# Optimization experiments

Hardware: AMD Instinct MI355X
Metric: run time of the kernel (lower is better)

Reference implementation:

```python
import jax, jax.numpy as jnp
import numpy as np

ALPHA = 0.2  # LeakyReLU slope in GAT
OUT_SLOPE = 0.01  # default nn.LeakyyReLU slope for self.out
B, E, IN_DIM, HID, HEADS = 4, 2048, 32, 18, 3
DH = HID // HEADS  # per-head out dim = 6


def _leaky(x, slope):
    return jnp.where(x > 0, x, slope * x)


def _gat_head(x, adj, W, a):
    # x: [B,E,in], W: [in,dh], a: [2*dh,1]
    h = jnp.einsum('bei,id->bed', x, W)                      # [B,E,dh]
    d = h.shape[-1]
    # score[b,i,j] = leakyrelu(a . concat(h_i, h_j)) = leakyrelu(h_i.a1 + h_j.a2)
    e1 = jnp.einsum('bed,d->be', h, a[:d, 0])
    e2 = jnp.einsum('bed,d->be', h, a[d:, 0])
    score = _leaky(e1[:, :, None] + e2[:, None, :], ALPHA)   # [B,E,E]
    scores = jnp.where(adj == 1.0, score, 0.0)
    logits = jnp.where(adj > 0.0, scores, -30.0)
    att = jax.nn.softmax(logits, axis=2)                     # softmax over j
    # h_prime[b,j,d] = sum_i att[b,i,j] * h[b,i,d]  (torch sums over dim=1)
    h_prime = jnp.einsum('bij,bid->bjd', att, h)
    return jax.nn.elu(h_prime)  # concat=True -> elu


def _gat_multihead(x, adj, Ws, As):
    # Ws: [H,in,dh], As: [H,2*dh,1]
    outs = jax.vmap(lambda W, a: _gat_head(x, adj, W, a))(Ws, As)  # [H,B,E,dh]
    H, b, e, d = outs.shape
    return jnp.moveaxis(outs, 0, 2).reshape(b, e, H * d)  # concat heads last-dim


def _gcn(x, adj2d, W, b):
    return adj2d @ (x @ W) + b


def setup_inputs() -> dict:
    key = jax.random.key(0)
    ks = jax.random.split(key, 16)
    node_input = jax.random.normal(ks[0], (B, E, IN_DIM), jnp.float32)
    uv_filed = jax.random.normal(ks[1], (B, E, IN_DIM), jnp.float32)
    adj = jax.random.randint(ks[2], (B, E, E), 0, 2).astype(jnp.float32)
    s = 0.1
    Wt1 = jax.random.normal(ks[3], (HEADS, IN_DIM, DH), jnp.float32) * s
    at1 = jax.random.normal(ks[4], (HEADS, 2 * DH, 1), jnp.float32) * s
    Wt2 = jax.random.normal(ks[5], (HEADS, IN_DIM, DH), jnp.float32) * s
    at2 = jax.random.normal(ks[6], (HEADS, 2 * DH, 1), jnp.float32) * s
    Wg1 = jax.random.normal(ks[7], (HID, 16), jnp.float32) * s
    bg1 = jnp.zeros((16,), jnp.float32)
    Wg2 = jax.random.normal(ks[8], (16, 2), jnp.float32) * s
    bg2 = jnp.zeros((2,), jnp.float32)
    Wo1 = jax.random.normal(ks[9], (HID, 16), jnp.float32) * s
    bo1 = jnp.zeros((16,), jnp.float32)
    Wo2 = jax.random.normal(ks[10], (16, 2), jnp.float32) * s
    bo2 = jnp.zeros((2,), jnp.float32)
    return dict(node_input=node_input, uv_filed=uv_filed, adj=adj,
                Wt1=Wt1, at1=at1, Wt2=Wt2, at2=at2,
                Wg1=Wg1, bg1=bg1, Wg2=Wg2, bg2=bg2,
                Wo1=Wo1, bo1=bo1, Wo2=Wo2, bo2=bo2)


def reference(node_input, uv_filed, adj, Wt1, at1, Wt2, at2,
              Wg1, bg1, Wg2, bg2, Wo1, bo1, Wo2, bo2):
    h = _gat_multihead(node_input, adj, Wt1, at1)  # [B,E,18]
    o = _gat_multihead(uv_filed, adj, Wt2, at2)    # [B,E,18]
    a0 = adj[0]
    Y = jax.nn.relu(_gcn(h[0], a0, Wg1, bg1))
    O = jax.nn.relu(_gcn(o[0], a0, Wo1, bo1))
    Y = _gcn(Y, a0, Wg2, bg2)
    O = _gcn(O, a0, Wo2, bo2)
    return (jax.nn.log_softmax(Y, axis=1), _leaky(O, OUT_SLOPE))
```

## Files before the change

kernel.cpp:

```cpp
#include <hip/hip_runtime.h>
#include <hip/hip_bf16.h>


__global__ __launch_bounds__(256) void k01(
    const float* __restrict__ adj0, unsigned int* __restrict__ bm,
    const float* __restrict__ node, const float* __restrict__ uv,
    const float* __restrict__ Wt1, const float* __restrict__ at1,
    const float* __restrict__ Wt2, const float* __restrict__ at2,
    float* __restrict__ hcol, float* __restrict__ pack1, float* __restrict__ pack2) {
  int b = blockIdx.x;
  if (b < 512) {
    int lane = threadIdx.x & 63, w = threadIdx.x >> 6;
    int row = b * 4 + w;
    const float* arow = adj0 + (size_t)row * 2048;
#pragma unroll 4
    for (int it = 0; it < 32; ++it) {
      float v = arow[it * 64 + lane];
      unsigned long long mask = __ballot(v == 1.0f);
      if (lane == 0) bm[row * 64 + it * 2] = (unsigned int)mask;
      else if (lane == 32) bm[row * 64 + it * 2 + 1] = (unsigned int)(mask >> 32);
    }
    return;
  }
  __shared__ float sW[192];
  __shared__ float sA[12];
  int fb = b - 512;
  int g = fb / 24;
  int h = (fb / 8) % 3;
  int e = (fb % 8) * 256 + threadIdx.x;
  const float* W = (g ? Wt2 : Wt1) + h * 192;
  const float* A = (g ? at2 : at1) + h * 12;
  const float* x = (g ? uv : node) + e * 32;
  if (threadIdx.x < 192) sW[threadIdx.x] = W[threadIdx.x];
  if (threadIdx.x < 12) sA[threadIdx.x] = A[threadIdx.x];
  __syncthreads();
  float xv[32];
#pragma unroll
  for (int i = 0; i < 32; ++i) xv[i] = x[i];
  float hv[6];
#pragma unroll
  for (int d = 0; d < 6; ++d) hv[d] = 0.f;
#pragma unroll
  for (int i = 0; i < 32; ++i)
#pragma unroll
    for (int d = 0; d < 6; ++d) hv[d] += xv[i] * sW[i * 6 + d];
  float e1 = 0.f, e2 = 0.f;
#pragma unroll
  for (int d = 0; d < 6; ++d) {
    e1 += hv[d] * sA[d];
    e2 += hv[d] * sA[6 + d];
  }
  int c = g * 3 + h;
#pragma unroll
  for (int d = 0; d < 6; ++d) hcol[(c * 6 + d) * 2048 + e] = hv[d];
  pack1[c * 2048 + e] = e1;
  pack1[(6 + c) * 2048 + e] = __expf(e1);
  pack1[(12 + c) * 2048 + e] = __expf(0.2f * e1);
  pack2[c * 2048 + e] = e2;
  pack2[(6 + c) * 2048 + e] = __expf(e2);
  pack2[(12 + c) * 2048 + e] = __expf(0.2f * e2);
}

__global__ __launch_bounds__(384) void k2_rowsum(
    const unsigned int* __restrict__ bm, const float* __restrict__ pack1,
    const float* __restrict__ pack2, const float* __restrict__ hcol,
    unsigned int* __restrict__ bmT, float* __restrict__ hsS) {
  int tid = threadIdx.x;
  int c = tid >> 6, lane = tid & 63;
  if (c < 4) {
    int t = blockIdx.x * 4 + c;
    int ti = t >> 5, tj = t & 31;
    const unsigned int* rw = &bm[(size_t)(ti * 64 + lane) * 64 + tj * 2];
    unsigned int rlo = rw[0], rhi = rw[1];
    unsigned long long rowbits = ((unsigned long long)rhi << 32) | rlo;
    unsigned int myLo = 0, myHi = 0;
#pragma unroll
    for (int jb = 0; jb < 64; ++jb) {
      unsigned long long colm = __ballot((unsigned int)((rowbits >> jb) & 1ull));
      if (jb == lane) { myLo = (unsigned int)colm; myHi = (unsigned int)(colm >> 32); }
    }
    *(uint2*)&bmT[(size_t)(tj * 64 + lane) * 64 + ti * 2] = make_uint2(myLo, myHi);
  }
  int i0 = blockIdx.x * 8;
  const float4* p2_4 = (const float4*)pack2;
  float e1r[8], p1r[8], q1r[8], sum[8];
#pragma unroll
  for (int r = 0; r < 8; ++r) {
    e1r[r] = pack1[c * 2048 + i0 + r];
    p1r[r] = pack1[(6 + c) * 2048 + i0 + r];
    q1r[r] = pack1[(12 + c) * 2048 + i0 + r];
    sum[r] = 0.f;
  }
  int sh = (lane & 7) * 4;
#pragma unroll
  for (int it = 0; it < 8; ++it) {
    int j4 = it * 64 + lane;
    float4 e2 = p2_4[c * 512 + j4];
    float4 p2 = p2_4[(6 + c) * 512 + j4];
    float4 q2 = p2_4[(12 + c) * 512 + j4];
    int wbase = it * 8 + (lane >> 3);
    float abx, aby, abz, abw;
#pragma unroll
    for (int r = 0; r < 8; ++r) {
      unsigned int wd = bm[(i0 + r) * 64 + wbase] >> sh;
      { float e = e1r[r] + e2.x; bool p = e > 0.f;
        abx = (p ? p1r[r] : q1r[r]) * (p ? p2.x : q2.x); }
      { float e = e1r[r] + e2.y; bool p = e > 0.f;
        aby = (p ? p1r[r] : q1r[r]) * (p ? p2.y : q2.y); }
      { float e = e1r[r] + e2.z; bool p = e > 0.f;
        abz = (p ? p1r[r] : q1r[r]) * (p ? p2.z : q2.z); }
      { float e = e1r[r] + e2.w; bool p = e > 0.f;
        abw = (p ? p1r[r] : q1r[r]) * (p ? p2.w : q2.w); }
      float s = ((wd & 1u) ? abx : 0.f) + ((wd & 2u) ? aby : 0.f) +
                ((wd & 4u) ? abz : 0.f) + ((wd & 8u) ? abw : 0.f);
      sum[r] += s;
    }
  }
#pragma unroll
  for (int r = 0; r < 8; ++r) {
#pragma unroll
    for (int off = 32; off > 0; off >>= 1) sum[r] += __shfl_xor(sum[r], off);
  }
  if (lane < 6) {
    int row = c * 6 + lane;
#pragma unroll
    for (int r = 0; r < 8; ++r) {
      float inv = 1.0f / sum[r];
      hsS[row * 2048 + i0 + r] = hcol[row * 2048 + i0 + r] * inv;
    }
  }
}

#define RLF(x, l) __int_as_float(__builtin_amdgcn_readlane(__float_as_int(x), (l)))
__global__ __launch_bounds__(384) void k3_hprime(
    const unsigned int* __restrict__ bmT, const float* __restrict__ pack1,
    const float* __restrict__ pack2, const float* __restrict__ hsS,
    float* __restrict__ hp_part) {
  int tid = threadIdx.x;
  int c = tid >> 6, jl = tid & 63;
  int j0 = blockIdx.x * 256;
  int i0 = blockIdx.y * 64;
  int il = i0 + jl;
  float e1L = pack1[c * 2048 + il];
  float p1L = pack1[(6 + c) * 2048 + il];
  float q1L = pack1[(12 + c) * 2048 + il];
  float hsL0 = hsS[(c * 6 + 0) * 2048 + il];
  float hsL1 = hsS[(c * 6 + 1) * 2048 + il];
  float hsL2 = hsS[(c * 6 + 2) * 2048 + il];
  float hsL3 = hsS[(c * 6 + 3) * 2048 + il];
  float hsL4 = hsS[(c * 6 + 4) * 2048 + il];
  float hsL5 = hsS[(c * 6 + 5) * 2048 + il];
  unsigned int cw0[4], cw1[4];
#pragma unroll
  for (int g = 0; g < 4; ++g) {
    uint2 w = *(const uint2*)&bmT[(size_t)(j0 + g * 64 + jl) * 64 + (i0 >> 5)];
    cw0[g] = w.x; cw1[g] = w.y;
  }
  float e2v[4], p2v[4], q2v[4];
#pragma unroll
  for (int g = 0; g < 4; ++g) {
    int j = j0 + g * 64 + jl;
    e2v[g] = pack2[c * 2048 + j];
    p2v[g] = pack2[(6 + c) * 2048 + j];
    q2v[g] = pack2[(12 + c) * 2048 + j];
  }
  float acc[4][6];
#pragma unroll
  for (int g = 0; g < 4; ++g)
#pragma unroll
    for (int d = 0; d < 6; ++d) acc[g][d] = 0.f;

#pragma unroll
  for (int half = 0; half < 2; ++half) {
#pragma unroll 8
    for (int i2 = 0; i2 < 32; ++i2) {
      int ii = half * 32 + i2;
      float e1 = RLF(e1L, ii);
      float p1 = RLF(p1L, ii);
      float q1 = RLF(q1L, ii);
      float h0 = RLF(hsL0, ii), h1 = RLF(hsL1, ii), h2 = RLF(hsL2, ii);
      float h3 = RLF(hsL3, ii), h4 = RLF(hsL4, ii), h5 = RLF(hsL5, ii);
#pragma unroll
      for (int g = 0; g < 4; ++g) {
        float e = e1 + e2v[g];
        bool pos = e > 0.f;
        float abp = p1 * p2v[g];
        float abq = q1 * q2v[g];
        float ab = pos ? abp : abq;
        unsigned int bit = ((half ? cw1[g] : cw0[g]) >> i2) & 1u;
        float wgt = bit ? ab : 0.f;
        acc[g][0] += wgt * h0; acc[g][1] += wgt * h1; acc[g][2] += wgt * h2;
        acc[g][3] += wgt * h3; acc[g][4] += wgt * h4; acc[g][5] += wgt * h5;
      }
    }
  }
  float* hp = hp_part + (size_t)blockIdx.y * 73728;
#pragma unroll
  for (int g = 0; g < 4; ++g) {
    int j = j0 + g * 64 + jl;
#pragma unroll
    for (int d = 0; d < 6; ++d) hp[(c * 6 + d) * 2048 + j] = acc[g][d];
  }
}

__global__ __launch_bounds__(256) void k4_T(
    const float* __restrict__ hp_part, const float* __restrict__ Wg1,
    const float* __restrict__ Wo1, float* __restrict__ T) {
  __shared__ float sHP[16 * 37];
  __shared__ float sWg[288], sWo[288];
  int tid = threadIdx.x;
  int j0 = blockIdx.x * 16;
  for (int idx = tid; idx < 288; idx += 256) {
    sWg[idx] = Wg1[idx];
    sWo[idx] = Wo1[idx];
  }
  for (int idx = tid; idx < 576; idx += 256) {
    int r = idx >> 4, jl = idx & 15;
    float s = 0.f;
#pragma unroll
    for (int sp = 0; sp < 32; ++sp)
      s += hp_part[(size_t)sp * 73728 + r * 2048 + j0 + jl];
    sHP[jl * 37 + r] = s;
  }
  __syncthreads();
  int jl = tid & 15, wq = tid >> 4;
  int gat = wq >> 3;
  int c0 = (wq & 7) * 2;
  const float* Wp = gat ? sWo : sWg;
  float a0 = 0.f, a1 = 0.f;
#pragma unroll
  for (int r = 0; r < 18; ++r) {
    float x = sHP[jl * 37 + gat * 18 + r];
    float hc = x > 0.f ? x : __expf(x) - 1.f;
    a0 += hc * Wp[r * 16 + c0];
    a1 += hc * Wp[r * 16 + c0 + 1];
  }
  T[(j0 + jl) * 32 + gat * 16 + c0] = a0;
  T[(j0 + jl) * 32 + gat * 16 + c0 + 1] = a1;
}

__global__ __launch_bounds__(256) void k5_gcn1(
    const unsigned int* __restrict__ bm, const float* __restrict__ T,
    float* __restrict__ Craw_part) {
  __shared__ unsigned int sM[64 * 4];
  __shared__ float4 sT4[128 * 8];
  const float4* T4 = (const float4*)T;
  int tid = threadIdx.x;
  int rl = tid & 31, cg = tid >> 5;
  int i0 = blockIdx.x * 64;
  int k0 = blockIdx.y * 128;
  sM[tid] = bm[(size_t)(i0 + (tid >> 2)) * 64 + (k0 >> 5) + (tid & 3)];
  for (int idx = tid; idx < 1024; idx += 256) sT4[idx] = T4[k0 * 8 + idx];
  __syncthreads();
  float a0x = 0.f, a0y = 0.f, a0z = 0.f, a0w = 0.f;
  float a1x = 0.f, a1y = 0.f, a1z = 0.f, a1w = 0.f;
#pragma unroll
  for (int wi = 0; wi < 4; ++wi) {
    unsigned int wA = sM[rl * 4 + wi];
    unsigned int wB = sM[(rl + 32) * 4 + wi];
#pragma unroll 16
    for (int kb = 0; kb < 32; ++kb) {
      float4 t = sT4[(wi * 32 + kb) * 8 + cg];
      float mA = (float)((wA >> kb) & 1u);
      float mB = (float)((wB >> kb) & 1u);
      a0x += mA * t.x; a0y += mA * t.y; a0z += mA * t.z; a0w += mA * t.w;
      a1x += mB * t.x; a1y += mB * t.y; a1z += mB * t.z; a1w += mB * t.w;
    }
  }
  float* base = Craw_part + (size_t)blockIdx.y * 65536;
  *(float4*)&base[(i0 + rl) * 32 + cg * 4] = make_float4(a0x, a0y, a0z, a0w);
  *(float4*)&base[(i0 + rl + 32) * 32 + cg * 4] = make_float4(a1x, a1y, a1z, a1w);
}

__global__ __launch_bounds__(256) void k6_T2(
    const float* __restrict__ Craw_part, const float* __restrict__ bg1,
    const float* __restrict__ Wg2, const float* __restrict__ bo1,
    const float* __restrict__ Wo2, float* __restrict__ T2) {
  int tid = threadIdx.x;
  int wave = tid >> 6, lane = tid & 63;
  int j = blockIdx.x * 8 + wave * 2 + (lane >> 5);
  int cl = lane & 31;
  int gat = cl >> 4, cc = cl & 15;
  float x = 0.f;
#pragma unroll
  for (int sp = 0; sp < 16; ++sp) x += Craw_part[(size_t)sp * 65536 + j * 32 + cl];
  x += gat ? bo1[cc] : bg1[cc];
  x = x > 0.f ? x : 0.f;
  float wa = gat ? Wo2[cc * 2 + 0] : Wg2[cc * 2 + 0];
  float wb = gat ? Wo2[cc * 2 + 1] : Wg2[cc * 2 + 1];
  float pa = x * wa, pb = x * wb;
#pragma unroll
  for (int m = 8; m > 0; m >>= 1) {
    pa += __shfl_xor(pa, m);
    pb += __shfl_xor(pb, m);
  }
  if (cc == 0) {
    T2[j * 4 + gat * 2 + 0] = pa;
    T2[j * 4 + gat * 2 + 1] = pb;
  }
}

__global__ __launch_bounds__(256) void k7_final(
    const unsigned int* __restrict__ bm, const float* __restrict__ T2,
    const float* __restrict__ bg2, const float* __restrict__ bo2,
    float* __restrict__ out) {
  int tid = threadIdx.x;
  int lane = tid & 63, w = tid >> 6;
  int r = blockIdx.x * 4 + w;
  const float4* T24 = (const float4*)T2;
  float4 acc = make_float4(0.f, 0.f, 0.f, 0.f);
  int sh = lane & 31;
#pragma unroll 8
  for (int it = 0; it < 32; ++it) {
    int k = it * 64 + lane;
    unsigned int wd = bm[r * 64 + it * 2 + (lane >> 5)];
    float m = (float)((wd >> sh) & 1u);
    float4 t = T24[k];
    acc.x += m * t.x;
    acc.y += m * t.y;
    acc.z += m * t.z;
    acc.w += m * t.w;
  }
#pragma unroll
  for (int off = 32; off > 0; off >>= 1) {
    acc.x += __shfl_down(acc.x, off);
    acc.y += __shfl_down(acc.y, off);
    acc.z += __shfl_down(acc.z, off);
    acc.w += __shfl_down(acc.w, off);
  }
  if (lane == 0) {
    float y0 = acc.x + bg2[0], y1 = acc.y + bg2[1];
    float m = fmaxf(y0, y1);
    float ls = m + logf(__expf(y0 - m) + __expf(y1 - m));
    out[r * 2 + 0] = y0 - ls;
    out[r * 2 + 1] = y1 - ls;
    float o0 = acc.z + bo2[0], o1 = acc.w + bo2[1];
    out[4096 + r * 2 + 0] = o0 > 0.f ? o0 : 0.01f * o0;
    out[4096 + r * 2 + 1] = o1 > 0.f ? o1 : 0.01f * o1;
  }
}

extern "C" void kernel_launch(void* const* d_in, const int* in_sizes, int n_in,
                              void* d_out, int out_size, void* d_ws, size_t ws_size,
                              hipStream_t stream) {
  const float* node = (const float*)d_in[0];
  const float* uv = (const float*)d_in[1];
  const float* adj = (const float*)d_in[2];
  const float* Wt1 = (const float*)d_in[3];
  const float* at1 = (const float*)d_in[4];
  const float* Wt2 = (const float*)d_in[5];
  const float* at2 = (const float*)d_in[6];
  const float* Wg1 = (const float*)d_in[7];
  const float* bg1 = (const float*)d_in[8];
  const float* Wg2 = (const float*)d_in[9];
  const float* bg2 = (const float*)d_in[10];
  const float* Wo1 = (const float*)d_in[11];
  const float* bo1 = (const float*)d_in[12];
  const float* Wo2 = (const float*)d_in[13];
  const float* bo2 = (const float*)d_in[14];
  float* ws = (float*)d_ws;
  float* hcol = ws;
  float* pack1 = ws + 73728;
  float* pack2 = ws + 110592;
  float* hsS = ws + 147456;
  float* T = ws + 221184;
  float* T2 = ws + 286720;
  unsigned int* bm = (unsigned int*)(ws + 294912);
  unsigned int* bmT = (unsigned int*)(ws + 425984);
  float* hp_part = ws + 557056;
  float* Craw_part = ws + 2916352;
  float* out = (float*)d_out;

  k01<<<560, 256, 0, stream>>>(adj, bm, node, uv, Wt1, at1, Wt2, at2,
                               hcol, pack1, pack2);
  k2_rowsum<<<256, 384, 0, stream>>>(bm, pack1, pack2, hcol, bmT, hsS);
  k3_hprime<<<dim3(8, 32), 384, 0, stream>>>(bmT, pack1, pack2, hsS, hp_part);
  k4_T<<<128, 256, 0, stream>>>(hp_part, Wg1, Wo1, T);
  k5_gcn1<<<dim3(32, 16), 256, 0, stream>>>(bm, T, Craw_part);
  k6_T2<<<256, 256, 0, stream>>>(Craw_part, bg1, Wg2, bo1, Wo2, T2);
  k7_final<<<512, 256, 0, stream>>>(bm, T2, bg2, bo2, out);
}
```

Baseline: 185.0 us.

## Fuse bitmask transpose into packing kernel and merge GAT/GCN stages into five kernels

```diff
diff --git a/kernel.cpp b/kernel.cpp
--- a/kernel.cpp
+++ b/kernel.cpp
@@ -2,29 +2,46 @@
 #include <hip/hip_bf16.h>
 
 
-__global__ __launch_bounds__(256) void k01(
+__global__ __launch_bounds__(256) void kA(
     const float* __restrict__ adj0, unsigned int* __restrict__ bm,
+    unsigned int* __restrict__ bmT,
     const float* __restrict__ node, const float* __restrict__ uv,
     const float* __restrict__ Wt1, const float* __restrict__ at1,
     const float* __restrict__ Wt2, const float* __restrict__ at2,
     float* __restrict__ hcol, float* __restrict__ pack1, float* __restrict__ pack2) {
   int b = blockIdx.x;
-  if (b < 512) {
+  if (b < 256) {
     int lane = threadIdx.x & 63, w = threadIdx.x >> 6;
-    int row = b * 4 + w;
-    const float* arow = adj0 + (size_t)row * 2048;
-#pragma unroll 4
-    for (int it = 0; it < 32; ++it) {
-      float v = arow[it * 64 + lane];
-      unsigned long long mask = __ballot(v == 1.0f);
-      if (lane == 0) bm[row * 64 + it * 2] = (unsigned int)mask;
-      else if (lane == 32) bm[row * 64 + it * 2 + 1] = (unsigned int)(mask >> 32);
-    }
+    int t = b * 4 + w;
+    int ti = t >> 5, tj = t & 31;
+    int row = ti * 64 + lane;
+    const float4* ar4 = (const float4*)(adj0 + (size_t)row * 2048 + tj * 64);
+    unsigned int rowLo = 0, rowHi = 0, myLo = 0, myHi = 0;
+#pragma unroll
+    for (int it = 0; it < 16; ++it) {
+      float4 v = ar4[it];
+      unsigned long long m0 = __ballot(v.x == 1.0f);
+      unsigned long long m1 = __ballot(v.y == 1.0f);
+      unsigned long long m2 = __ballot(v.z == 1.0f);
+      unsigned long long m3 = __ballot(v.w == 1.0f);
+      int jb = it * 4;
+      if (jb + 0 == lane) { myLo = (unsigned int)m0; myHi = (unsigned int)(m0 >> 32); }
+      if (jb + 1 == lane) { myLo = (unsigned int)m1; myHi = (unsigned int)(m1 >> 32); }
+      if (jb + 2 == lane) { myLo = (unsigned int)m2; myHi = (unsigned int)(m2 >> 32); }
+      if (jb + 3 == lane) { myLo = (unsigned int)m3; myHi = (unsigned int)(m3 >> 32); }
+      unsigned int rb = (v.x == 1.0f ? 1u : 0u) | (v.y == 1.0f ? 2u : 0u) |
+                        (v.z == 1.0f ? 4u : 0u) | (v.w == 1.0f ? 8u : 0u);
+      if (it < 8) rowLo |= rb << (it * 4);
+      else rowHi |= rb << ((it - 8) * 4);
+    }
+    *(uint2*)&bm[(size_t)row * 64 + tj * 2] = make_uint2(rowLo, rowHi);
+    int j = tj * 64 + lane;
+    *(uint2*)&bmT[(size_t)j * 64 + ti * 2] = make_uint2(myLo, myHi);
     return;
   }
   __shared__ float sW[192];
   __shared__ float sA[12];
-  int fb = b - 512;
+  int fb = b - 256;
   int g = fb / 24;
   int h = (fb / 8) % 3;
   int e = (fb % 8) * 256 + threadIdx.x;
@@ -61,26 +78,12 @@
   pack2[(12 + c) * 2048 + e] = __expf(0.2f * e2);
 }
 
-__global__ __launch_bounds__(384) void k2_rowsum(
+__global__ __launch_bounds__(384) void kB(
     const unsigned int* __restrict__ bm, const float* __restrict__ pack1,
     const float* __restrict__ pack2, const float* __restrict__ hcol,
-    unsigned int* __restrict__ bmT, float* __restrict__ hsS) {
+    float* __restrict__ hsS) {
   int tid = threadIdx.x;
   int c = tid >> 6, lane = tid & 63;
-  if (c < 4) {
-    int t = blockIdx.x * 4 + c;
-    int ti = t >> 5, tj = t & 31;
-    const unsigned int* rw = &bm[(size_t)(ti * 64 + lane) * 64 + tj * 2];
-    unsigned int rlo = rw[0], rhi = rw[1];
-    unsigned long long rowbits = ((unsigned long long)rhi << 32) | rlo;
-    unsigned int myLo = 0, myHi = 0;
-#pragma unroll
-    for (int jb = 0; jb < 64; ++jb) {
-      unsigned long long colm = __ballot((unsigned int)((rowbits >> jb) & 1ull));
-      if (jb == lane) { myLo = (unsigned int)colm; myHi = (unsigned int)(colm >> 32); }
-    }
-    *(uint2*)&bmT[(size_t)(tj * 64 + lane) * 64 + ti * 2] = make_uint2(myLo, myHi);
-  }
   int i0 = blockIdx.x * 8;
   const float4* p2_4 = (const float4*)pack2;
   float e1r[8], p1r[8], q1r[8], sum[8];
@@ -131,176 +134,173 @@
   }
 }
 
-#define RLF(x, l) __int_as_float(__builtin_amdgcn_readlane(__float_as_int(x), (l)))
-__global__ __launch_bounds__(384) void k3_hprime(
+__global__ __launch_bounds__(384) void kC(
     const unsigned int* __restrict__ bmT, const float* __restrict__ pack1,
     const float* __restrict__ pack2, const float* __restrict__ hsS,
-    float* __restrict__ hp_part) {
+    const float* __restrict__ Wg1, const float* __restrict__ Wo1,
+    float* __restrict__ T) {
+  __shared__ float sW[576];
+  __shared__ float sHP[4 * 37];
   int tid = threadIdx.x;
-  int c = tid >> 6, jl = tid & 63;
-  int j0 = blockIdx.x * 256;
-  int i0 = blockIdx.y * 64;
-  int il = i0 + jl;
-  float e1L = pack1[c * 2048 + il];
-  float p1L = pack1[(6 + c) * 2048 + il];
-  float q1L = pack1[(12 + c) * 2048 + il];
-  float hsL0 = hsS[(c * 6 + 0) * 2048 + il];
-  float hsL1 = hsS[(c * 6 + 1) * 2048 + il];
-  float hsL2 = hsS[(c * 6 + 2) * 2048 + il];
-  float hsL3 = hsS[(c * 6 + 3) * 2048 + il];
-  float hsL4 = hsS[(c * 6 + 4) * 2048 + il];
-  float hsL5 = hsS[(c * 6 + 5) * 2048 + il];
-  unsigned int cw0[4], cw1[4];
-#pragma unroll
-  for (int g = 0; g < 4; ++g) {
-    uint2 w = *(const uint2*)&bmT[(size_t)(j0 + g * 64 + jl) * 64 + (i0 >> 5)];
-    cw0[g] = w.x; cw1[g] = w.y;
-  }
+  int c = tid >> 6, L = tid & 63;
+  int j0 = blockIdx.x * 4;
+  if (tid < 288) { sW[tid] = Wg1[tid]; sW[288 + tid] = Wo1[tid]; }
+  int wj[4];
+#pragma unroll
+  for (int jj = 0; jj < 4; ++jj) wj[jj] = (int)bmT[(size_t)(j0 + jj) * 64 + L];
   float e2v[4], p2v[4], q2v[4];
 #pragma unroll
-  for (int g = 0; g < 4; ++g) {
-    int j = j0 + g * 64 + jl;
-    e2v[g] = pack2[c * 2048 + j];
-    p2v[g] = pack2[(6 + c) * 2048 + j];
-    q2v[g] = pack2[(12 + c) * 2048 + j];
+  for (int jj = 0; jj < 4; ++jj) {
+    e2v[jj] = pack2[c * 2048 + j0 + jj];
+    p2v[jj] = pack2[(6 + c) * 2048 + j0 + jj];
+    q2v[jj] = pack2[(12 + c) * 2048 + j0 + jj];
   }
   float acc[4][6];
 #pragma unroll
-  for (int g = 0; g < 4; ++g)
-#pragma unroll
-    for (int d = 0; d < 6; ++d) acc[g][d] = 0.f;
-
-#pragma unroll
-  for (int half = 0; half < 2; ++half) {
-#pragma unroll 8
-    for (int i2 = 0; i2 < 32; ++i2) {
-      int ii = half * 32 + i2;
-      float e1 = RLF(e1L, ii);
-      float p1 = RLF(p1L, ii);
-      float q1 = RLF(q1L, ii);
-      float h0 = RLF(hsL0, ii), h1 = RLF(hsL1, ii), h2 = RLF(hsL2, ii);
-      float h3 = RLF(hsL3, ii), h4 = RLF(hsL4, ii), h5 = RLF(hsL5, ii);
-#pragma unroll
-      for (int g = 0; g < 4; ++g) {
-        float e = e1 + e2v[g];
-        bool pos = e > 0.f;
-        float abp = p1 * p2v[g];
-        float abq = q1 * q2v[g];
-        float ab = pos ? abp : abq;
-        unsigned int bit = ((half ? cw1[g] : cw0[g]) >> i2) & 1u;
-        float wgt = bit ? ab : 0.f;
-        acc[g][0] += wgt * h0; acc[g][1] += wgt * h1; acc[g][2] += wgt * h2;
-        acc[g][3] += wgt * h3; acc[g][4] += wgt * h4; acc[g][5] += wgt * h5;
+  for (int jj = 0; jj < 4; ++jj)
+#pragma unroll
+    for (int d = 0; d < 6; ++d) acc[jj][d] = 0.f;
+
+  for (int s = 0; s < 32; ++s) {
+    int i = s * 64 + L;
+    float e1 = pack1[c * 2048 + i];
+    float p1 = pack1[(6 + c) * 2048 + i];
+    float q1 = pack1[(12 + c) * 2048 + i];
+    float h0 = hsS[(c * 6 + 0) * 2048 + i];
+    float h1 = hsS[(c * 6 + 1) * 2048 + i];
+    float h2 = hsS[(c * 6 + 2) * 2048 + i];
+    float h3 = hsS[(c * 6 + 3) * 2048 + i];
+    float h4 = hsS[(c * 6 + 4) * 2048 + i];
+    float h5 = hsS[(c * 6 + 5) * 2048 + i];
+#pragma unroll
+    for (int jj = 0; jj < 4; ++jj) {
+      int lo = __builtin_amdgcn_readlane(wj[jj], 2 * s);
+      int hi = __builtin_amdgcn_readlane(wj[jj], 2 * s + 1);
+      unsigned int wsel = (unsigned int)((L & 32) ? hi : lo);
+      float e = e1 + e2v[jj];
+      bool pos = e > 0.f;
+      float ab = (pos ? p1 : q1) * (pos ? p2v[jj] : q2v[jj]);
+      float wgt = ((wsel >> (L & 31)) & 1u) ? ab : 0.f;
+      acc[jj][0] += wgt * h0; acc[jj][1] += wgt * h1; acc[jj][2] += wgt * h2;
+      acc[jj][3] += wgt * h3; acc[jj][4] += wgt * h4; acc[jj][5] += wgt * h5;
+    }
+  }
+#pragma unroll
+  for (int jj = 0; jj < 4; ++jj)
+#pragma unroll
+    for (int d = 0; d < 6; ++d)
+#pragma unroll
+      for (int off = 32; off > 0; off >>= 1)
+        acc[jj][d] += __shfl_xor(acc[jj][d], off);
+  if (L == 0) {
+#pragma unroll
+    for (int jj = 0; jj < 4; ++jj)
+#pragma unroll
+      for (int d = 0; d < 6; ++d) {
+        float x = acc[jj][d];
+        sHP[jj * 37 + c * 6 + d] = x > 0.f ? x : __expf(x) - 1.f;
       }
-    }
-  }
-  float* hp = hp_part + (size_t)blockIdx.y * 73728;
-#pragma unroll
-  for (int g = 0; g < 4; ++g) {
-    int j = j0 + g * 64 + jl;
-#pragma unroll
-    for (int d = 0; d < 6; ++d) hp[(c * 6 + d) * 2048 + j] = acc[g][d];
-  }
-}
-
-__global__ __launch_bounds__(256) void k4_T(
-    const float* __restrict__ hp_part, const float* __restrict__ Wg1,
-    const float* __restrict__ Wo1, float* __restrict__ T) {
-  __shared__ float sHP[16 * 37];
-  __shared__ float sWg[288], sWo[288];
+  }
+  __syncthreads();
+  if (tid < 128) {
+    int j = tid >> 5, col = tid & 31;
+    int gat = col >> 4, cp = col & 15;
+    const float* Wp = sW + gat * 288;
+    const float* hp = sHP + j * 37 + gat * 18;
+    float a = 0.f;
+#pragma unroll
+    for (int r = 0; r < 18; ++r) a += hp[r] * Wp[r * 16 + cp];
+    T[(size_t)(j0 + j) * 32 + col] = a;
+  }
+}
+
+__global__ __launch_bounds__(256) void kD(
+    const unsigned int* __restrict__ bm, const float* __restrict__ T,
+    const float* __restrict__ bg1, const float* __restrict__ bo1,
+    const float* __restrict__ Wg2, const float* __restrict__ Wo2,
+    float* __restrict__ T2) {
+  __shared__ float sC[8 * 32];
   int tid = threadIdx.x;
-  int j0 = blockIdx.x * 16;
-  for (int idx = tid; idx < 288; idx += 256) {
-    sWg[idx] = Wg1[idx];
-    sWo[idx] = Wo1[idx];
-  }
-  for (int idx = tid; idx < 576; idx += 256) {
-    int r = idx >> 4, jl = idx & 15;
-    float s = 0.f;
-#pragma unroll
-    for (int sp = 0; sp < 32; ++sp)
-      s += hp_part[(size_t)sp * 73728 + r * 2048 + j0 + jl];
-    sHP[jl * 37 + r] = s;
+  int kl = tid & 31, cg = tid >> 5;
+  int r0 = blockIdx.x * 8;
+  const float4* T4 = (const float4*)T;
+  float4 acc[8];
+#pragma unroll
+  for (int rr = 0; rr < 8; ++rr) acc[rr] = make_float4(0.f, 0.f, 0.f, 0.f);
+  for (int ch = 0; ch < 8; ++ch) {
+    float4 tv[8];
+#pragma unroll
+    for (int t = 0; t < 8; ++t)
+      tv[t] = T4[(size_t)(ch * 256 + t * 32 + kl) * 8 + cg];
+#pragma unroll
+    for (int rr = 0; rr < 8; ++rr) {
+      const unsigned int* wp = &bm[(size_t)(r0 + rr) * 64 + ch * 8];
+      uint4 wA = *(const uint4*)wp;
+      uint4 wB = *(const uint4*)(wp + 4);
+      float m;
+      m = (float)((wA.x >> kl) & 1u);
+      acc[rr].x += m * tv[0].x; acc[rr].y += m * tv[0].y;
+      acc[rr].z += m * tv[0].z; acc[rr].w += m * tv[0].w;
+      m = (float)((wA.y >> kl) & 1u);
+      acc[rr].x += m * tv[1].x; acc[rr].y += m * tv[1].y;
+      acc[rr].z += m * tv[1].z; acc[rr].w += m * tv[1].w;
+      m = (float)((wA.z >> kl) & 1u);
+      acc[rr].x += m * tv[2].x; acc[rr].y += m * tv[2].y;
+      acc[rr].z += m * tv[2].z; acc[rr].w += m * tv[2].w;
+      m = (float)((wA.w >> kl) & 1u);
+      acc[rr].x += m * tv[3].x; acc[rr].y += m * tv[3].y;
+      acc[rr].z += m * tv[3].z; acc[rr].w += m * tv[3].w;
+      m = (float)((wB.x >> kl) & 1u);
+      acc[rr].x += m * tv[4].x; acc[rr].y += m * tv[4].y;
+      acc[rr].z += m * tv[4].z; acc[rr].w += m * tv[4].w;
+      m = (float)((wB.y >> kl) & 1u);
+      acc[rr].x += m * tv[5].x; acc[rr].y += m * tv[5].y;
+      acc[rr].z += m * tv[5].z; acc[rr].w += m * tv[5].w;
+      m = (float)((wB.z >> kl) & 1u);
+      acc[rr].x += m * tv[6].x; acc[rr].y += m * tv[6].y;
+      acc[rr].z += m * tv[6].z; acc[rr].w += m * tv[6].w;
+      m = (float)((wB.w >> kl) & 1u);
+      acc[rr].x += m * tv[7].x; acc[rr].y += m * tv[7].y;
+      acc[rr].z += m * tv[7].z; acc[rr].w += m * tv[7].w;
+    }
+  }
+#pragma unroll
+  for (int rr = 0; rr < 8; ++rr) {
+#pragma unroll
+    for (int m = 16; m > 0; m >>= 1) {
+      acc[rr].x += __shfl_xor(acc[rr].x, m);
+      acc[rr].y += __shfl_xor(acc[rr].y, m);
+      acc[rr].z += __shfl_xor(acc[rr].z, m);
+      acc[rr].w += __shfl_xor(acc[rr].w, m);
+    }
+  }
+  if (kl == 0) {
+#pragma unroll
+    for (int rr = 0; rr < 8; ++rr)
+      *(float4*)&sC[rr * 32 + cg * 4] = acc[rr];
   }
   __syncthreads();
-  int jl = tid & 15, wq = tid >> 4;
-  int gat = wq >> 3;
-  int c0 = (wq & 7) * 2;
-  const float* Wp = gat ? sWo : sWg;
-  float a0 = 0.f, a1 = 0.f;
-#pragma unroll
-  for (int r = 0; r < 18; ++r) {
-    float x = sHP[jl * 37 + gat * 18 + r];
-    float hc = x > 0.f ? x : __expf(x) - 1.f;
-    a0 += hc * Wp[r * 16 + c0];
-    a1 += hc * Wp[r * 16 + c0 + 1];
-  }
-  T[(j0 + jl) * 32 + gat * 16 + c0] = a0;
-  T[(j0 + jl) * 32 + gat * 16 + c0 + 1] = a1;
-}
-
-__global__ __launch_bounds__(256) void k5_gcn1(
-    const unsigned int* __restrict__ bm, const float* __restrict__ T,
-    float* __restrict__ Craw_part) {
-  __shared__ unsigned int sM[64 * 4];
-  __shared__ float4 sT4[128 * 8];
-  const float4* T4 = (const float4*)T;
-  int tid = threadIdx.x;
-  int rl = tid & 31, cg = tid >> 5;
-  int i0 = blockIdx.x * 64;
-  int k0 = blockIdx.y * 128;
-  sM[tid] = bm[(size_t)(i0 + (tid >> 2)) * 64 + (k0 >> 5) + (tid & 3)];
-  for (int idx = tid; idx < 1024; idx += 256) sT4[idx] = T4[k0 * 8 + idx];
-  __syncthreads();
-  float a0x = 0.f, a0y = 0.f, a0z = 0.f, a0w = 0.f;
-  float a1x = 0.f, a1y = 0.f, a1z = 0.f, a1w = 0.f;
-#pragma unroll
-  for (int wi = 0; wi < 4; ++wi) {
-    unsigned int wA = sM[rl * 4 + wi];
-    unsigned int wB = sM[(rl + 32) * 4 + wi];
-#pragma unroll 16
-    for (int kb = 0; kb < 32; ++kb) {
-      float4 t = sT4[(wi * 32 + kb) * 8 + cg];
-      float mA = (float)((wA >> kb) & 1u);
-      float mB = (float)((wB >> kb) & 1u);
-      a0x += mA * t.x; a0y += mA * t.y; a0z += mA * t.z; a0w += mA * t.w;
-      a1x += mB * t.x; a1y += mB * t.y; a1z += mB * t.z; a1w += mB * t.w;
-    }
-  }
-  float* base = Craw_part + (size_t)blockIdx.y * 65536;
-  *(float4*)&base[(i0 + rl) * 32 + cg * 4] = make_float4(a0x, a0y, a0z, a0w);
-  *(float4*)&base[(i0 + rl + 32) * 32 + cg * 4] = make_float4(a1x, a1y, a1z, a1w);
-}
-
-__global__ __launch_bounds__(256) void k6_T2(
-    const float* __restrict__ Craw_part, const float* __restrict__ bg1,
-    const float* __restrict__ Wg2, const float* __restrict__ bo1,
-    const float* __restrict__ Wo2, float* __restrict__ T2) {
-  int tid = threadIdx.x;
-  int wave = tid >> 6, lane = tid & 63;
-  int j = blockIdx.x * 8 + wave * 2 + (lane >> 5);
-  int cl = lane & 31;
-  int gat = cl >> 4, cc = cl & 15;
-  float x = 0.f;
-#pragma unroll
-  for (int sp = 0; sp < 16; ++sp) x += Craw_part[(size_t)sp * 65536 + j * 32 + cl];
-  x += gat ? bo1[cc] : bg1[cc];
-  x = x > 0.f ? x : 0.f;
-  float wa = gat ? Wo2[cc * 2 + 0] : Wg2[cc * 2 + 0];
-  float wb = gat ? Wo2[cc * 2 + 1] : Wg2[cc * 2 + 1];
-  float pa = x * wa, pb = x * wb;
-#pragma unroll
-  for (int m = 8; m > 0; m >>= 1) {
-    pa += __shfl_xor(pa, m);
-    pb += __shfl_xor(pb, m);
-  }
-  if (cc == 0) {
-    T2[j * 4 + gat * 2 + 0] = pa;
-    T2[j * 4 + gat * 2 + 1] = pb;
-  }
-}
-
-__global__ __launch_bounds__(256) void k7_final(
+  {
+    int r = tid >> 5, col = tid & 31;
+    int gat = col >> 4, cc = col & 15;
+    float x = sC[r * 32 + col] + (gat ? bo1[cc] : bg1[cc]);
+    x = x > 0.f ? x : 0.f;
+    float wa = gat ? Wo2[cc * 2 + 0] : Wg2[cc * 2 + 0];
+    float wb = gat ? Wo2[cc * 2 + 1] : Wg2[cc * 2 + 1];
+    float pa = x * wa, pb = x * wb;
+#pragma unroll
+    for (int m = 8; m > 0; m >>= 1) {
+      pa += __shfl_xor(pa, m);
+      pb += __shfl_xor(pb, m);
+    }
+    if (cc == 0) {
+      T2[(size_t)(r0 + r) * 4 + gat * 2 + 0] = pa;
+      T2[(size_t)(r0 + r) * 4 + gat * 2 + 1] = pb;
+    }
+  }
+}
+
+__global__ __launch_bounds__(256) void kE(
     const unsigned int* __restrict__ bm, const float* __restrict__ T2,
     const float* __restrict__ bg2, const float* __restrict__ bo2,
     float* __restrict__ out) {
@@ -367,16 +367,12 @@
   float* T2 = ws + 286720;
   unsigned int* bm = (unsigned int*)(ws + 294912);
   unsigned int* bmT = (unsigned int*)(ws + 425984);
-  float* hp_part = ws + 557056;
-  float* Craw_part = ws + 2916352;
   float* out = (float*)d_out;
 
-  k01<<<560, 256, 0, stream>>>(adj, bm, node, uv, Wt1, at1, Wt2, at2,
-                               hcol, pack1, pack2);
-  k2_rowsum<<<256, 384, 0, stream>>>(bm, pack1, pack2, hcol, bmT, hsS);
-  k3_hprime<<<dim3(8, 32), 384, 0, stream>>>(bmT, pack1, pack2, hsS, hp_part);
-  k4_T<<<128, 256, 0, stream>>>(hp_part, Wg1, Wo1, T);
-  k5_gcn1<<<dim3(32, 16), 256, 0, stream>>>(bm, T, Craw_part);
-  k6_T2<<<256, 256, 0, stream>>>(Craw_part, bg1, Wg2, bo1, Wo2, T2);
-  k7_final<<<512, 256, 0, stream>>>(bm, T2, bg2, bo2, out);
-}
+  kA<<<304, 256, 0, stream>>>(adj, bm, bmT, node, uv, Wt1, at1, Wt2, at2,
+                              hcol, pack1, pack2);
+  kB<<<256, 384, 0, stream>>>(bm, pack1, pack2, hcol, hsS);
+  kC<<<512, 384, 0, stream>>>(bmT, pack1, pack2, hsS, Wg1, Wo1, T);
+  kD<<<256, 256, 0, stream>>>(bm, T, bg1, bo1, Wg2, Wo2, T2);
+  kE<<<512, 256, 0, stream>>>(bm, T2, bg2, bo2, out);
+}
```

Result: faster. 171.2 us (median of 3 runs) (-7.5%).
